# Optimization experiments

Measured on AMD Instinct MI355X. Metric: run time of the kernel, lower is better.

The kernel has to match this reference:

```python
import jax, jax.numpy as jnp
import numpy as np

DIM_OUT = 64


def setup_inputs() -> dict:
    key = jax.random.key(0)
    k1, k2, k3, k4 = jax.random.split(key, 4)
    B, N, D_in, D_out = 4, 4096, 512, DIM_OUT
    x = jax.random.normal(k1, (B, N, D_in), dtype=jnp.float32)
    s = 1.0 / np.sqrt(D_in)
    Wk = jax.random.normal(k2, (D_out, D_in), dtype=jnp.float32) * s
    Wq = jax.random.normal(k3, (D_out, D_in), dtype=jnp.float32) * s
    Wv = jax.random.normal(k4, (D_out, D_in), dtype=jnp.float32) * s
    return {"x": x, "Wk": Wk, "Wq": Wq, "Wv": Wv}


def reference(x, Wk, Wq, Wv):
    # x: [B, N, D_in]; W*: [D_out, D_in] (torch Linear, no bias -> x @ W.T)
    keys = jnp.einsum('bnd,od->bno', x, Wk)
    queries = jnp.einsum('bnd,od->bno', x, Wq)
    values = jnp.einsum('bnd,od->bno', x, Wv)
    d_out = Wk.shape[0]
    # causal attention scores: [B, N, N]
    scores = jnp.einsum('bio,bjo->bij', queries, keys) / jnp.sqrt(jnp.float32(d_out))
    N = x.shape[1]
    causal = jnp.tril(jnp.ones((N, N), dtype=bool))  # [N, N]
    scores = jnp.where(causal[None, :, :], scores, -jnp.inf)
    att = jax.nn.softmax(scores, axis=-1)
    return jnp.einsum('bjo,bij->bio', values, att)
```

## Files before the change

### kernel.cpp

```cpp
#include <hip/hip_runtime.h>
#include <hip/hip_bf16.h>
#include <math.h>

#define N_   4096
#define DIN  512
#define D_   64

typedef __attribute__((ext_vector_type(8))) short  bf16x8;
typedef __attribute__((ext_vector_type(4))) float  f32x4;

__device__ __forceinline__ unsigned short bf16rne(float x) {
    unsigned u = __float_as_uint(x);
    return (unsigned short)((u + 0x7FFFu + ((u >> 16) & 1u)) >> 16);
}
__device__ __forceinline__ unsigned cvt2(float a, float b) {
    __hip_bfloat162 h = __float22bfloat162_rn(make_float2(a, b));
    unsigned u; __builtin_memcpy(&u, &h, 4);
    return u;
}
__device__ __forceinline__ uint2 cvt4(float4 v) {
    return make_uint2(cvt2(v.x, v.y), cvt2(v.z, v.w));
}

__device__ __forceinline__ int pb64(int qi) {
    const int k = qi >> 4;
    return qi + 16 * (k * (k - 1) / 2) + (qi & 15) * k;
}

#define PART64_F 4160

__global__ __launch_bounds__(512) void proj_kernel(
    const float* __restrict__ X, const float* __restrict__ Wk,
    const float* __restrict__ Wq, const float* __restrict__ Wv,
    unsigned short* __restrict__ Kb, unsigned short* __restrict__ Qb,
    unsigned short* __restrict__ Vt)
{
    __shared__ unsigned short Xs[2][64 * 72];
    __shared__ unsigned short Ws[2][192 * 72];

    const int tid  = threadIdx.x;
    const int lane = tid & 63;
    const int w    = tid >> 6;
    const int q15  = lane & 15;
    const int hi   = lane >> 4;
    const int rt   = w >> 1;
    const int oh   = w & 1;
    const int rbase = blockIdx.x * 64;

    float4 xr[2], wr[6];

    auto loadT = [&](int kc) {
        #pragma unroll
        for (int i = 0; i < 2; ++i) {
            const int idx = tid + i * 512;
            xr[i] = *(const float4*)(X + (size_t)(rbase + (idx >> 4)) * DIN + kc + (idx & 15) * 4);
        }
        #pragma unroll
        for (int i = 0; i < 6; ++i) {
            const int idx  = tid + i * 512;
            const int wrow = idx >> 4;
            const float* Wp = (wrow < 64)  ? Wk + (size_t)wrow * DIN
                            : (wrow < 128) ? Wq + (size_t)(wrow - 64) * DIN
                                           : Wv + (size_t)(wrow - 128) * DIN;
            wr[i] = *(const float4*)(Wp + kc + (idx & 15) * 4);
        }
    };
    auto storeT = [&](int p) {
        #pragma unroll
        for (int i = 0; i < 2; ++i) {
            const int idx = tid + i * 512;
            *(uint2*)&Xs[p][(idx >> 4) * 72 + (idx & 15) * 4] = cvt4(xr[i]);
        }
        #pragma unroll
        for (int i = 0; i < 6; ++i) {
            const int idx = tid + i * 512;
            *(uint2*)&Ws[p][(idx >> 4) * 72 + (idx & 15) * 4] = cvt4(wr[i]);
        }
    };

    f32x4 acc[6];
    #pragma unroll
    for (int i = 0; i < 6; ++i) acc[i] = (f32x4){0.f, 0.f, 0.f, 0.f};

    loadT(0);
    int p = 0;
    for (int it = 0; it < 8; ++it) {
        storeT(p);
        __syncthreads();
        if (it < 7) loadT((it + 1) * 64);
        #pragma unroll
        for (int ks = 0; ks < 2; ++ks) {
            bf16x8 af = *(const bf16x8*)&Xs[p][(rt * 16 + q15) * 72 + ks * 32 + hi * 8];
            #pragma unroll
            for (int j = 0; j < 6; ++j) {
                bf16x8 bfr = *(const bf16x8*)&Ws[p][((oh * 6 + j) * 16 + q15) * 72 + ks * 32 + hi * 8];
                acc[j] = __builtin_amdgcn_mfma_f32_16x16x32_bf16(af, bfr, acc[j], 0, 0, 0);
            }
        }
        p ^= 1;
    }

    unsigned short* Os = &Ws[0][0];
    #pragma unroll
    for (int j = 0; j < 6; ++j) {
        const int og = oh * 6 + j;
        #pragma unroll
        for (int r = 0; r < 4; ++r) {
            const int n = rt * 16 + hi * 4 + r;
            const int o = og * 16 + q15;
            unsigned short v = bf16rne(acc[j][r]);
            if (og < 4)      Kb[(size_t)(rbase + n) * D_ + o]        = v;
            else if (og < 8) Qb[(size_t)(rbase + n) * D_ + (o - 64)] = v;
            else             Os[n * 66 + (o - 128)]                  = v;
        }
    }
    __syncthreads();
    {
        const int o  = tid >> 3;
        const int ng = (tid & 7) * 8;
        unsigned short tmp[8];
        #pragma unroll
        for (int i = 0; i < 8; ++i) tmp[i] = Os[(ng + i) * 66 + o];
        const int b  = rbase >> 12;
        const int nb = rbase & (N_ - 1);
        *(uint4*)(Vt + ((size_t)b * D_ + o) * N_ + nb + ng) = *(uint4*)&tmp[0];
    }
}

__global__ __launch_bounds__(256, 3) void attn_part_kernel(
    const unsigned short* __restrict__ Qb, const unsigned short* __restrict__ Kb,
    const unsigned short* __restrict__ Vt, float* __restrict__ Pws)
{
    __shared__ unsigned short Ks[2][64 * 72];
    __shared__ unsigned short Vs[2][64 * 72];
    __shared__ unsigned short Pb[4][16 * 72];

    const int tid  = threadIdx.x;
    const int lane = tid & 63;
    const int w    = tid >> 6;
    const int q15  = lane & 15;
    const int hi   = lane >> 4;

    const int b  = blockIdx.x & 3;
    const int qi = (blockIdx.x >> 2) & 63;
    const int sl = blockIdx.x >> 8;
    const int nch  = qi + 1;
    const int cbeg = sl * 16;
    if (cbeg >= nch) return;
    const int cend = min(nch, cbeg + 16);

    const unsigned short* Qp = Qb + (size_t)b * N_ * D_;
    const unsigned short* Kp = Kb + (size_t)b * N_ * D_;
    const unsigned short* Vp = Vt + (size_t)b * D_ * N_;

    const int qg = qi * 64 + w * 16 + q15;
    bf16x8 qf[2];
    #pragma unroll
    for (int ks = 0; ks < 2; ++ks)
        qf[ks] = *(const bf16x8*)(Qp + (size_t)qg * D_ + ks * 32 + hi * 8);

    f32x4 accO[4];
    #pragma unroll
    for (int dt = 0; dt < 4; ++dt) accO[dt] = (f32x4){0.f, 0.f, 0.f, 0.f};
    float lsum = 0.f;

    const int srow = tid >> 2;
    const int se0  = (tid & 3) * 16;
    uint4 kr0, kr1, vr0, vr1;

    auto loadC = [&](int c) {
        const int kb2 = c * 64;
        const unsigned short* kp = Kp + (size_t)(kb2 + srow) * D_ + se0;
        kr0 = *(const uint4*)kp;
        kr1 = *(const uint4*)(kp + 8);
        const unsigned short* vp = Vp + (size_t)srow * N_ + kb2 + se0;
        vr0 = *(const uint4*)vp;
        vr1 = *(const uint4*)(vp + 8);
    };
    auto writeC = [&](int p) {
        *(uint4*)&Ks[p][srow * 72 + se0]     = kr0;
        *(uint4*)&Ks[p][srow * 72 + se0 + 8] = kr1;
        *(uint4*)&Vs[p][srow * 72 + se0]     = vr0;
        *(uint4*)&Vs[p][srow * 72 + se0 + 8] = vr1;
    };

    loadC(cbeg);
    writeC(0);
    __syncthreads();

    unsigned short* Pw = &Pb[w][0];
    const float SC = 0.125f * 1.44269504f;
    int p = 0;

    for (int c = cbeg; c < cend; ++c) {
        const int kbase = c * 64;
        if (c + 1 < cend) loadC(c + 1);

        f32x4 sv[4];
        #pragma unroll
        for (int kt = 0; kt < 4; ++kt) {
            bf16x8 k0 = *(const bf16x8*)&Ks[p][(kt * 16 + q15) * 72 + hi * 8];
            bf16x8 k1 = *(const bf16x8*)&Ks[p][(kt * 16 + q15) * 72 + 32 + hi * 8];
            sv[kt] = __builtin_amdgcn_mfma_f32_16x16x32_bf16(k0, qf[0], (f32x4){0.f,0.f,0.f,0.f}, 0, 0, 0);
            sv[kt] = __builtin_amdgcn_mfma_f32_16x16x32_bf16(k1, qf[1], sv[kt], 0, 0, 0);
        }

        #pragma unroll
        for (int kt = 0; kt < 4; ++kt) {
            float pv[4];
            #pragma unroll
            for (int r = 0; r < 4; ++r) {
                float v = sv[kt][r] * SC;
                const int kg = kbase + kt * 16 + hi * 4 + r;
                v = (kg <= qg) ? v : -INFINITY;
                pv[r] = __builtin_amdgcn_exp2f(v);
                lsum += pv[r];
            }
            *(uint2*)&Pw[q15 * 72 + kt * 16 + hi * 4] =
                make_uint2(cvt2(pv[0], pv[1]), cvt2(pv[2], pv[3]));
        }

        #pragma unroll
        for (int ks2 = 0; ks2 < 2; ++ks2) {
            bf16x8 pf = *(const bf16x8*)&Pw[q15 * 72 + ks2 * 32 + hi * 8];
            #pragma unroll
            for (int dt = 0; dt < 4; ++dt) {
                bf16x8 vf = *(const bf16x8*)&Vs[p][(dt * 16 + q15) * 72 + ks2 * 32 + hi * 8];
                accO[dt] = __builtin_amdgcn_mfma_f32_16x16x32_bf16(vf, pf, accO[dt], 0, 0, 0);
            }
        }

        __syncthreads();
        if (c + 1 < cend) writeC(p ^ 1);
        __syncthreads();
        p ^= 1;
    }

    lsum += __shfl_xor(lsum, 16);
    lsum += __shfl_xor(lsum, 32);

    float* partO = Pws + ((size_t)b * 160 + pb64(qi) + sl) * PART64_F;
    #pragma unroll
    for (int dt = 0; dt < 4; ++dt)
        #pragma unroll
        for (int r = 0; r < 4; ++r)
            partO[(dt * 16 + hi * 4 + r) * 64 + w * 16 + q15] = accO[dt][r];
    if (hi == 0) partO[4096 + w * 16 + q15] = lsum;
}

__global__ __launch_bounds__(256) void attn_merge_kernel(
    const float* __restrict__ Pws, float* __restrict__ O)
{
    __shared__ float Tr[64 * 68];
    __shared__ float Ls[64];

    const int tid = threadIdx.x;
    const int b   = blockIdx.x & 3;
    const int qi  = blockIdx.x >> 2;
    const int np  = (qi + 16) >> 4;
    const float* base = Pws + ((size_t)b * 160 + pb64(qi)) * PART64_F;

    {
        const int d  = tid >> 2;
        const int qg = (tid & 3) * 16;
        float s[16];
        #pragma unroll
        for (int i = 0; i < 16; ++i) s[i] = 0.f;
        for (int pp = 0; pp < np; ++pp) {
            const float* sp = base + (size_t)pp * PART64_F + d * 64 + qg;
            #pragma unroll
            for (int i = 0; i < 4; ++i) {
                float4 v = *(const float4*)(sp + i * 4);
                s[4*i]   += v.x; s[4*i+1] += v.y;
                s[4*i+2] += v.z; s[4*i+3] += v.w;
            }
        }
        #pragma unroll
        for (int i = 0; i < 16; ++i) Tr[d * 68 + qg + i] = s[i];
    }
    if (tid < 64) {
        float L = 0.f;
        for (int pp = 0; pp < np; ++pp) L += base[(size_t)pp * PART64_F + 4096 + tid];
        Ls[tid] = 1.0f / L;
    }
    __syncthreads();
    {
        const int q  = tid >> 2;
        const int dg = (tid & 3) * 16;
        const float rL = Ls[q];
        float ov[16];
        #pragma unroll
        for (int i = 0; i < 16; ++i) ov[i] = Tr[(dg + i) * 68 + q] * rL;
        float* dst = O + ((size_t)b * N_ + qi * 64 + q) * D_ + dg;
        #pragma unroll
        for (int i = 0; i < 4; ++i)
            *(float4*)(dst + i * 4) = make_float4(ov[4*i], ov[4*i+1], ov[4*i+2], ov[4*i+3]);
    }
}

extern "C" void kernel_launch(void* const* d_in, const int* in_sizes, int n_in,
                              void* d_out, int out_size, void* d_ws, size_t ws_size,
                              hipStream_t stream)
{
    const float* x  = (const float*)d_in[0];
    const float* Wk = (const float*)d_in[1];
    const float* Wq = (const float*)d_in[2];
    const float* Wv = (const float*)d_in[3];
    float* O = (float*)d_out;

    const size_t per = (size_t)4 * N_ * D_;
    unsigned short* Kb = (unsigned short*)d_ws;
    unsigned short* Qb = Kb + per;
    unsigned short* Vt = Qb + per;
    float* Pws = (float*)((char*)d_ws + 3 * per * sizeof(unsigned short));

    proj_kernel<<<dim3(4 * N_ / 64), 512, 0, stream>>>(x, Wk, Wq, Wv, Kb, Qb, Vt);
    attn_part_kernel<<<dim3(1024), 256, 0, stream>>>(Qb, Kb, Vt, Pws);
    attn_merge_kernel<<<dim3(256), 256, 0, stream>>>(Pws, O);
}
```

Before: 53.21 us.

## Swizzle LDS tiles instead of padding and compact attention grid heaviest-first

Replaces the padded 72-element LDS row stride with a 64-element stride plus an XOR swizzle on 16-byte chunks, in both the projection and attention kernels. This is meant to avoid bank conflicts while using less shared memory. The attention grid drops from 1024 to 640 blocks by enumerating only valid (slice, query-tile) pairs, with the largest query tiles scheduled first, so no blocks launch just to exit early and the load is better balanced. This relies on the new block-index mapping matching the partial-result indexing in the merge kernel.

```diff
diff --git a/kernel.cpp b/kernel.cpp
--- a/kernel.cpp
+++ b/kernel.cpp
@@ -20,6 +20,9 @@
 }
 __device__ __forceinline__ uint2 cvt4(float4 v) {
     return make_uint2(cvt2(v.x, v.y), cvt2(v.z, v.w));
+}
+__device__ __forceinline__ int swz(int row, int byte_in_row) {
+    return (row * 128 + (byte_in_row ^ ((row & 7) << 4))) >> 1;
 }
 
 __device__ __forceinline__ int pb64(int qi) {
@@ -35,8 +38,8 @@
     unsigned short* __restrict__ Kb, unsigned short* __restrict__ Qb,
     unsigned short* __restrict__ Vt)
 {
-    __shared__ unsigned short Xs[2][64 * 72];
-    __shared__ unsigned short Ws[2][192 * 72];
+    __shared__ unsigned short Xs[2][64 * 64];
+    __shared__ unsigned short Ws[2][192 * 64];
 
     const int tid  = threadIdx.x;
     const int lane = tid & 63;
@@ -69,12 +72,12 @@
         #pragma unroll
         for (int i = 0; i < 2; ++i) {
             const int idx = tid + i * 512;
-            *(uint2*)&Xs[p][(idx >> 4) * 72 + (idx & 15) * 4] = cvt4(xr[i]);
+            *(uint2*)&Xs[p][swz(idx >> 4, (idx & 15) * 8)] = cvt4(xr[i]);
         }
         #pragma unroll
         for (int i = 0; i < 6; ++i) {
             const int idx = tid + i * 512;
-            *(uint2*)&Ws[p][(idx >> 4) * 72 + (idx & 15) * 4] = cvt4(wr[i]);
+            *(uint2*)&Ws[p][swz(idx >> 4, (idx & 15) * 8)] = cvt4(wr[i]);
         }
     };
 
@@ -90,10 +93,10 @@
         if (it < 7) loadT((it + 1) * 64);
         #pragma unroll
         for (int ks = 0; ks < 2; ++ks) {
-            bf16x8 af = *(const bf16x8*)&Xs[p][(rt * 16 + q15) * 72 + ks * 32 + hi * 8];
+            bf16x8 af = *(const bf16x8*)&Xs[p][swz(rt * 16 + q15, ks * 64 + hi * 16)];
             #pragma unroll
             for (int j = 0; j < 6; ++j) {
-                bf16x8 bfr = *(const bf16x8*)&Ws[p][((oh * 6 + j) * 16 + q15) * 72 + ks * 32 + hi * 8];
+                bf16x8 bfr = *(const bf16x8*)&Ws[p][swz((oh * 6 + j) * 16 + q15, ks * 64 + hi * 16)];
                 acc[j] = __builtin_amdgcn_mfma_f32_16x16x32_bf16(af, bfr, acc[j], 0, 0, 0);
             }
         }
@@ -131,9 +134,9 @@
     const unsigned short* __restrict__ Qb, const unsigned short* __restrict__ Kb,
     const unsigned short* __restrict__ Vt, float* __restrict__ Pws)
 {
-    __shared__ unsigned short Ks[2][64 * 72];
-    __shared__ unsigned short Vs[2][64 * 72];
-    __shared__ unsigned short Pb[4][16 * 72];
+    __shared__ unsigned short Ks[2][64 * 64];
+    __shared__ unsigned short Vs[2][64 * 64];
+    __shared__ unsigned short Pb[4][16 * 64];
 
     const int tid  = threadIdx.x;
     const int lane = tid & 63;
@@ -141,12 +144,15 @@
     const int q15  = lane & 15;
     const int hi   = lane >> 4;
 
-    const int b  = blockIdx.x & 3;
-    const int qi = (blockIdx.x >> 2) & 63;
-    const int sl = blockIdx.x >> 8;
+    const int b = blockIdx.x & 3;
+    const int u = blockIdx.x >> 2;
+    int sl, qi;
+    if      (u < 64)  { sl = 0; qi = 63 - u; }
+    else if (u < 112) { sl = 1; qi = 63 - (u - 64); }
+    else if (u < 144) { sl = 2; qi = 63 - (u - 112); }
+    else              { sl = 3; qi = 63 - (u - 144); }
     const int nch  = qi + 1;
     const int cbeg = sl * 16;
-    if (cbeg >= nch) return;
     const int cend = min(nch, cbeg + 16);
 
     const unsigned short* Qp = Qb + (size_t)b * N_ * D_;
@@ -165,23 +171,23 @@
     float lsum = 0.f;
 
     const int srow = tid >> 2;
-    const int se0  = (tid & 3) * 16;
+    const int sb0  = (tid & 3) * 32;
     uint4 kr0, kr1, vr0, vr1;
 
     auto loadC = [&](int c) {
         const int kb2 = c * 64;
-        const unsigned short* kp = Kp + (size_t)(kb2 + srow) * D_ + se0;
+        const unsigned short* kp = Kp + (size_t)(kb2 + srow) * D_ + sb0 / 2;
         kr0 = *(const uint4*)kp;
         kr1 = *(const uint4*)(kp + 8);
-        const unsigned short* vp = Vp + (size_t)srow * N_ + kb2 + se0;
+        const unsigned short* vp = Vp + (size_t)srow * N_ + kb2 + sb0 / 2;
         vr0 = *(const uint4*)vp;
         vr1 = *(const uint4*)(vp + 8);
     };
     auto writeC = [&](int p) {
-        *(uint4*)&Ks[p][srow * 72 + se0]     = kr0;
-        *(uint4*)&Ks[p][srow * 72 + se0 + 8] = kr1;
-        *(uint4*)&Vs[p][srow * 72 + se0]     = vr0;
-        *(uint4*)&Vs[p][srow * 72 + se0 + 8] = vr1;
+        *(uint4*)&Ks[p][swz(srow, sb0)]      = kr0;
+        *(uint4*)&Ks[p][swz(srow, sb0 + 16)] = kr1;
+        *(uint4*)&Vs[p][swz(srow, sb0)]      = vr0;
+        *(uint4*)&Vs[p][swz(srow, sb0 + 16)] = vr1;
     };
 
     loadC(cbeg);
@@ -199,8 +205,8 @@
         f32x4 sv[4];
         #pragma unroll
         for (int kt = 0; kt < 4; ++kt) {
-            bf16x8 k0 = *(const bf16x8*)&Ks[p][(kt * 16 + q15) * 72 + hi * 8];
-            bf16x8 k1 = *(const bf16x8*)&Ks[p][(kt * 16 + q15) * 72 + 32 + hi * 8];
+            bf16x8 k0 = *(const bf16x8*)&Ks[p][swz(kt * 16 + q15, hi * 16)];
+            bf16x8 k1 = *(const bf16x8*)&Ks[p][swz(kt * 16 + q15, 64 + hi * 16)];
             sv[kt] = __builtin_amdgcn_mfma_f32_16x16x32_bf16(k0, qf[0], (f32x4){0.f,0.f,0.f,0.f}, 0, 0, 0);
             sv[kt] = __builtin_amdgcn_mfma_f32_16x16x32_bf16(k1, qf[1], sv[kt], 0, 0, 0);
         }
@@ -216,16 +222,16 @@
                 pv[r] = __builtin_amdgcn_exp2f(v);
                 lsum += pv[r];
             }
-            *(uint2*)&Pw[q15 * 72 + kt * 16 + hi * 4] =
+            *(uint2*)&Pw[swz(q15, kt * 32 + hi * 8)] =
                 make_uint2(cvt2(pv[0], pv[1]), cvt2(pv[2], pv[3]));
         }
 
         #pragma unroll
         for (int ks2 = 0; ks2 < 2; ++ks2) {
-            bf16x8 pf = *(const bf16x8*)&Pw[q15 * 72 + ks2 * 32 + hi * 8];
+            bf16x8 pf = *(const bf16x8*)&Pw[swz(q15, ks2 * 64 + hi * 16)];
             #pragma unroll
             for (int dt = 0; dt < 4; ++dt) {
-                bf16x8 vf = *(const bf16x8*)&Vs[p][(dt * 16 + q15) * 72 + ks2 * 32 + hi * 8];
+                bf16x8 vf = *(const bf16x8*)&Vs[p][swz(dt * 16 + q15, ks2 * 64 + hi * 16)];
                 accO[dt] = __builtin_amdgcn_mfma_f32_16x16x32_bf16(vf, pf, accO[dt], 0, 0, 0);
             }
         }
@@ -315,6 +321,6 @@
     float* Pws = (float*)((char*)d_ws + 3 * per * sizeof(unsigned short));
 
     proj_kernel<<<dim3(4 * N_ / 64), 512, 0, stream>>>(x, Wk, Wq, Wv, Kb, Qb, Vt);
-    attn_part_kernel<<<dim3(1024), 256, 0, stream>>>(Qb, Kb, Vt, Pws);
+    attn_part_kernel<<<dim3(640), 256, 0, stream>>>(Qb, Kb, Vt, Pws);
     attn_merge_kernel<<<dim3(256), 256, 0, stream>>>(Pws, O);
 }
```

Measured after the change: 51.56 us. -3.1%, faster.
